# Optimization experiments

Measured on AMD Instinct MI355X. Metric: run time of the kernel, lower is better.

## Reference

```python
import jax, jax.numpy as jnp
import numpy as np

N_NODES = 50000
N_EDGES = 400000
D = 300          # num_features == hidden_units
L = 5            # num_layers
C = 128          # num_outputs
NG = 256         # graphs per batch
BN_EPS = 1e-5


def setup_inputs() -> dict:
    key = jax.random.key(0)
    ks = jax.random.split(key, 16)
    x = jax.random.normal(ks[0], (N_NODES, D), dtype=jnp.float32)
    edge_index = jax.random.randint(ks[1], (2, N_EDGES), 0, N_NODES, dtype=jnp.int64)
    batch = jnp.sort(jax.random.randint(ks[2], (N_NODES,), 0, NG, dtype=jnp.int64))
    s = 1.0 / np.sqrt(D)
    # Stacked per-layer GINConv MLP params: Linear -> BN -> ReLU -> Linear, then outer BN
    mlp_W1 = jax.random.uniform(ks[3], (L, D, D), jnp.float32, -s, s)
    mlp_b1 = jax.random.uniform(ks[4], (L, D), jnp.float32, -s, s)
    mlp_g1 = jnp.ones((L, D), jnp.float32)
    mlp_be1 = jnp.zeros((L, D), jnp.float32)
    mlp_W2 = jax.random.uniform(ks[5], (L, D, D), jnp.float32, -s, s)
    mlp_b2 = jax.random.uniform(ks[6], (L, D), jnp.float32, -s, s)
    bn_g = jnp.ones((L, D), jnp.float32)
    bn_b = jnp.zeros((L, D), jnp.float32)
    # num_layers+1 readout heads (num_features == hidden_units so all [D, C])
    fc_W = jax.random.uniform(ks[7], (L + 1, D, C), jnp.float32, -s, s)
    fc_b = jax.random.uniform(ks[8], (L + 1, C), jnp.float32, -s, s)
    return dict(x=x, edge_index=edge_index, batch=batch,
                mlp_W1=mlp_W1, mlp_b1=mlp_b1, mlp_g1=mlp_g1, mlp_be1=mlp_be1,
                mlp_W2=mlp_W2, mlp_b2=mlp_b2, bn_g=bn_g, bn_b=bn_b,
                fc_W=fc_W, fc_b=fc_b)


def _bn(h, gamma, beta):
    # BatchNorm1d in training mode: biased batch stats over the node dim
    mu = h.mean(axis=0)
    var = h.var(axis=0)
    return (h - mu) * jax.lax.rsqrt(var + BN_EPS) * gamma + beta


def reference(x, edge_index, batch, mlp_W1, mlp_b1, mlp_g1, mlp_be1,
              mlp_W2, mlp_b2, bn_g, bn_b, fc_W, fc_b):
    src, dst = edge_index[0], edge_index[1]
    n = x.shape[0]
    outs = [x]
    h = x
    for i in range(L):
        # GINConv (eps=0): MLP(x + sum_{j in N(i)} x_j), scatter-add over edges
        agg = jax.ops.segment_sum(h[src], dst, num_segments=n)
        z = h + agg
        z = z @ mlp_W1[i] + mlp_b1[i]
        z = jax.nn.relu(_bn(z, mlp_g1[i], mlp_be1[i]))
        z = z @ mlp_W2[i] + mlp_b2[i]
        h = jax.nn.relu(_bn(z, bn_g[i], bn_b[i]))  # outer BN + ReLU
        outs.append(h)
    # global mean pool per graph, then per-depth linear heads summed (dropout off in eval)
    counts = jax.ops.segment_sum(jnp.ones((n,), x.dtype), batch, num_segments=NG)
    inv = 1.0 / jnp.maximum(counts, 1.0)
    out = jnp.zeros((NG, C), x.dtype)
    for i, hi in enumerate(outs):
        pooled = jax.ops.segment_sum(hi, batch, num_segments=NG) * inv[:, None]
        out = out + (pooled @ fc_W[i] + fc_b[i])
    return out
```

## Files before the change

kernel.cpp:

```cpp
#include <hip/hip_runtime.h>

#define D 300
#define KP 320
#define NPAD 50048
#define NT128 391
#define WSTRIDE 328
#define NGR 256
#define NL 5
#define NC 128
#define SPART 8
#define BN_EPS 1e-5f

typedef __attribute__((ext_vector_type(8))) short bf16x8;
typedef __attribute__((ext_vector_type(4))) float f32x4;
typedef unsigned short u16;

__device__ __forceinline__ void atomAdd(float* p, float v) { unsafeAtomicAdd(p, v); }

__device__ __forceinline__ short f2bf(float f) {
    union { float f; unsigned u; } v; v.f = f;
    unsigned r = v.u + 0x7fffu + ((v.u >> 16) & 1u);
    return (short)(r >> 16);
}
__device__ __forceinline__ float bf2f(short s) {
    union { unsigned u; float f; } v;
    v.u = ((unsigned)(u16)s) << 16;
    return v.f;
}
__device__ __forceinline__ unsigned cvtpk(float lo, float hi) {
    unsigned r;
    asm("v_cvt_pk_bf16_f32 %0, %1, %2" : "=v"(r) : "v"(lo), "v"(hi));
    return r;
}
template<int C>
__device__ __forceinline__ float rs_add(float v) {
    int x = __builtin_amdgcn_update_dpp(0, __float_as_int(v), C, 0xF, 0xF, true);
    return v + __int_as_float(x);
}
__device__ __forceinline__ float red16(float v) {
    v = rs_add<0x111>(v);
    v = rs_add<0x112>(v);
    v = rs_add<0x114>(v);
    v = rs_add<0x118>(v);
    return v;
}

__global__ void offsets_kernel(const int* __restrict__ batch, int* __restrict__ off, int N) {
    int g = threadIdx.x;
    if (g > NGR) return;
    int lo = 0, hi = N;
    while (lo < hi) {
        int mid = (lo + hi) >> 1;
        if (batch[mid] < g) lo = mid + 1; else hi = mid;
    }
    off[g] = lo;
}

__global__ __launch_bounds__(256)
void deg_kernel(const int* __restrict__ ei, int* __restrict__ deg, int E) {
    int e = blockIdx.x * 256 + threadIdx.x;
    if (e < E) atomicAdd(&deg[ei[E + e]], 1);
}

__global__ __launch_bounds__(256)
void degpart_kernel(const int* __restrict__ deg, int* __restrict__ part, int N) {
    int i = blockIdx.x * 256 + threadIdx.x;
    int v = (i < N) ? deg[i] : 0;
    #pragma unroll
    for (int o = 1; o < 64; o <<= 1) v += __shfl_xor(v, o);
    __shared__ int ws[4];
    if ((threadIdx.x & 63) == 0) ws[threadIdx.x >> 6] = v;
    __syncthreads();
    if (threadIdx.x == 0) part[blockIdx.x] = ws[0] + ws[1] + ws[2] + ws[3];
}

__global__ __launch_bounds__(256)
void partscan_kernel(int* __restrict__ part, int nb) {
    __shared__ int buf[256];
    int t = threadIdx.x;
    int v = (t < nb) ? part[t] : 0;
    buf[t] = v;
    __syncthreads();
    for (int o = 1; o < 256; o <<= 1) {
        int u = (t >= o) ? buf[t - o] : 0;
        __syncthreads();
        buf[t] += u;
        __syncthreads();
    }
    if (t < nb) part[t] = (t == 0) ? 0 : buf[t - 1];
}

__global__ __launch_bounds__(256)
void rowptr_kernel(const int* __restrict__ deg, const int* __restrict__ part,
                   int* __restrict__ rowptr, int N, int E) {
    __shared__ int buf[256];
    int b = blockIdx.x, t = threadIdx.x;
    int i = b * 256 + t;
    int v = (i < N) ? deg[i] : 0;
    buf[t] = v;
    __syncthreads();
    for (int o = 1; o < 256; o <<= 1) {
        int u = (t >= o) ? buf[t - o] : 0;
        __syncthreads();
        buf[t] += u;
        __syncthreads();
    }
    if (i < N) rowptr[i] = part[b] + buf[t] - v;
    if (b == 0 && t == 0) rowptr[N] = E;
}

__global__ __launch_bounds__(256)
void fill_kernel(const int* __restrict__ ei, const int* __restrict__ rowptr,
                 int* __restrict__ cursor, int* __restrict__ col, int E) {
    int e = blockIdx.x * 256 + threadIdx.x;
    if (e >= E) return;
    int src = ei[e];
    int dst = ei[E + e];
    int pos = atomicAdd(&cursor[dst], 1);
    col[rowptr[dst] + pos] = src;
}

__global__ __launch_bounds__(256)
void wcvt_kernel(const float* __restrict__ W1, const float* __restrict__ W2,
                 u16* __restrict__ Wt) {
    int idx = blockIdx.x * 256 + threadIdx.x;
    if (idx >= 10 * KP * 80) return;
    int n4 = idx % 80;
    int k = (idx / 80) % KP;
    int mat = idx / (80 * KP);
    const float* Wsrc = (mat < NL) ? (W1 + (size_t)mat * D * D) : (W2 + (size_t)(mat - NL) * D * D);
    float4 w = make_float4(0.f, 0.f, 0.f, 0.f);
    if (k < D && n4 < 75) w = *(const float4*)(Wsrc + (size_t)k * D + n4 * 4);
    size_t base = ((size_t)mat * 320 + n4 * 4) * KP + k;
    Wt[base]          = (u16)f2bf(w.x);
    Wt[base + KP]     = (u16)f2bf(w.y);
    Wt[base + 2 * KP] = (u16)f2bf(w.z);
    Wt[base + 3 * KP] = (u16)f2bf(w.w);
}

__global__ __launch_bounds__(256)
void xcvt_kernel(const float* __restrict__ x, u16* __restrict__ xbf, int N) {
    int idx = blockIdx.x * 256 + threadIdx.x;
    if (idx >= NPAD * 40) return;
    int row = idx / 40;
    int c8 = (idx - row * 40) * 8;
    short o[8];
    #pragma unroll
    for (int i = 0; i < 8; ++i) {
        int c = c8 + i;
        float f = (row < N && c < D) ? x[(size_t)row * D + c] : 0.f;
        o[i] = f2bf(f);
    }
    *(bf16x8*)(xbf + (size_t)row * KP + c8) = *(bf16x8*)o;
}

template<bool APPLY>
__global__ __launch_bounds__(256)
void gather_kernel(const u16* __restrict__ H, u16* __restrict__ Z,
                   const int* __restrict__ rowptr, const int* __restrict__ col,
                   const float* __restrict__ scsh, int N) {
    int idx = blockIdx.x * 256 + threadIdx.x;
    if (idx >= N * 40) return;
    int node = idx / 40;
    int c8 = (idx - node * 40) * 8;
    float sc[8], sh[8];
    if (APPLY) {
        #pragma unroll
        for (int i = 0; i < 8; ++i) { sc[i] = scsh[c8 + i]; sh[i] = scsh[KP + c8 + i]; }
    }
    int s = rowptr[node], e = rowptr[node + 1];
    bf16x8 v = *(const bf16x8*)(H + (size_t)node * KP + c8);
    float acc[8];
    #pragma unroll
    for (int i = 0; i < 8; ++i) {
        float f = bf2f(v[i]);
        acc[i] = APPLY ? fmaxf(fmaf(f, sc[i], sh[i]), 0.f) : f;
    }
    int j = s;
    for (; j + 2 <= e; j += 2) {
        int s0 = col[j], s1 = col[j + 1];
        bf16x8 w0 = *(const bf16x8*)(H + (size_t)s0 * KP + c8);
        bf16x8 w1 = *(const bf16x8*)(H + (size_t)s1 * KP + c8);
        #pragma unroll
        for (int i = 0; i < 8; ++i) {
            float f0 = bf2f(w0[i]);
            float f1 = bf2f(w1[i]);
            acc[i] += APPLY ? fmaxf(fmaf(f0, sc[i], sh[i]), 0.f) : f0;
            acc[i] += APPLY ? fmaxf(fmaf(f1, sc[i], sh[i]), 0.f) : f1;
        }
    }
    if (j < e) {
        int s0 = col[j];
        bf16x8 w0 = *(const bf16x8*)(H + (size_t)s0 * KP + c8);
        #pragma unroll
        for (int i = 0; i < 8; ++i) {
            float f0 = bf2f(w0[i]);
            acc[i] += APPLY ? fmaxf(fmaf(f0, sc[i], sh[i]), 0.f) : f0;
        }
    }
    short o[8];
    #pragma unroll
    for (int i = 0; i < 8; ++i) o[i] = f2bf(acc[i]);
    *(bf16x8*)(Z + (size_t)node * KP + c8) = *(bf16x8*)o;
}

template<bool APPLY>
__global__ __launch_bounds__(320)
void pool_kernel(const u16* __restrict__ H, const int* __restrict__ off,
                 const float* __restrict__ scsh, float* __restrict__ pooled_l) {
    __shared__ float red[8][KP];
    int t = threadIdx.x;
    int g = blockIdx.x;
    int rq = t / 40;
    int c8 = (t - rq * 40) * 8;
    float sc[8], sh[8];
    if (APPLY) {
        #pragma unroll
        for (int i = 0; i < 8; ++i) { sc[i] = scsh[c8 + i]; sh[i] = scsh[KP + c8 + i]; }
    }
    int r0 = off[g], r1 = off[g + 1];
    float a[8] = {};
    for (int r = r0 + rq; r < r1; r += 8) {
        bf16x8 v = *(const bf16x8*)(H + (size_t)r * KP + c8);
        #pragma unroll
        for (int i = 0; i < 8; ++i) {
            float f = bf2f(v[i]);
            a[i] += APPLY ? fmaxf(fmaf(f, sc[i], sh[i]), 0.f) : f;
        }
    }
    #pragma unroll
    for (int i = 0; i < 8; ++i) red[rq][c8 + i] = a[i];
    __syncthreads();
    int c = t;
    if (c < D) {
        float s = 0.f;
        #pragma unroll
        for (int j = 0; j < 8; ++j) s += red[j][c];
        pooled_l[g * D + c] = s;
    }
}

template<bool APPLY>
__global__ __launch_bounds__(256, 3)
void mfma_gemm_kernel(const u16* __restrict__ Abf, const u16* __restrict__ Wt,
                      const float* __restrict__ scsh,
                      u16* __restrict__ Cbf, float* __restrict__ stats, int Nreal) {
    __shared__ u16 Ws[80 * WSTRIDE];
    __shared__ float lsum[80], lsq[80];
    const int tid = threadIdx.x;
    const int bid = blockIdx.x;
    const int xcd = bid & 7;
    const int pos = bid >> 3;
    const int tile = xcd + ((pos >> 2) << 3);
    const int nBase = (pos & 3) * 80;
    if (tile >= NT128) return;
    const int wave = tid >> 6, lane = tid & 63;
    const int quad = lane >> 4, l16 = lane & 15;

    const u16* pA = Abf + (size_t)(tile * 128 + wave * 16 + l16) * KP + quad * 8;
    bf16x8 a[2][10];
    #pragma unroll
    for (int kc = 0; kc < 10; ++kc) {
        a[0][kc] = *(const bf16x8*)(pA + kc * 32);
        a[1][kc] = *(const bf16x8*)(pA + (size_t)64 * KP + kc * 32);
    }

    {
        const u16* src = Wt + (size_t)nBase * KP;
        for (int unit = tid; unit < 80 * 40; unit += 256) {
            int n = unit / 40, kg = unit - n * 40;
            int kc = kg >> 2, q = kg & 3;
            *(bf16x8*)&Ws[n * WSTRIDE + kc * 32 + ((q ^ (n & 3)) << 3)] =
                *(const bf16x8*)(src + (size_t)n * KP + kg * 8);
        }
    }
    if (tid < 80) { lsum[tid] = 0.f; lsq[tid] = 0.f; }

    #pragma unroll
    for (int kc = 0; kc < 10; ++kc) {
        asm volatile("" : "+v"(a[0][kc]));
        asm volatile("" : "+v"(a[1][kc]));
    }
    __syncthreads();

    if (APPLY) {
        #pragma unroll
        for (int kc = 0; kc < 10; ++kc) {
            const float* sp = scsh + kc * 32 + quad * 8;
            float4 s0 = *(const float4*)sp;
            float4 s1 = *(const float4*)(sp + 4);
            float4 h0 = *(const float4*)(sp + KP);
            float4 h1 = *(const float4*)(sp + KP + 4);
            float sc[8] = {s0.x, s0.y, s0.z, s0.w, s1.x, s1.y, s1.z, s1.w};
            float sh[8] = {h0.x, h0.y, h0.z, h0.w, h1.x, h1.y, h1.z, h1.w};
            #pragma unroll
            for (int g = 0; g < 2; ++g) {
                float f[8];
                #pragma unroll
                for (int i = 0; i < 8; ++i)
                    f[i] = fmaxf(fmaf(bf2f(a[g][kc][i]), sc[i], sh[i]), 0.f);
                union { unsigned u[4]; bf16x8 v; } o;
                o.u[0] = cvtpk(f[0], f[1]);
                o.u[1] = cvtpk(f[2], f[3]);
                o.u[2] = cvtpk(f[4], f[5]);
                o.u[3] = cvtpk(f[6], f[7]);
                a[g][kc] = o.v;
            }
        }
    }

    int wb[5];
    #pragma unroll
    for (int nt = 0; nt < 5; ++nt)
        wb[nt] = (nt * 16 + l16) * WSTRIDE + ((quad ^ (l16 & 3)) << 3);

    f32x4 acc[2][5] = {};
    __builtin_amdgcn_s_setprio(1);
    #pragma unroll
    for (int kc = 0; kc < 10; ++kc) {
        #pragma unroll
        for (int nt = 0; nt < 5; ++nt) {
            bf16x8 b = *(const bf16x8*)&Ws[wb[nt] + kc * 32];
            acc[0][nt] = __builtin_amdgcn_mfma_f32_16x16x32_bf16(b, a[0][kc], acc[0][nt], 0, 0, 0);
            acc[1][nt] = __builtin_amdgcn_mfma_f32_16x16x32_bf16(b, a[1][kc], acc[1][nt], 0, 0, 0);
        }
    }
    __builtin_amdgcn_s_setprio(0);

    const int r0g = tile * 128 + wave * 16 + l16;
    const bool ok0 = r0g < Nreal, ok1 = (r0g + 64) < Nreal;
    u16* crow0 = Cbf + (size_t)r0g * KP + nBase + quad * 4;
    u16* crow1 = crow0 + (size_t)64 * KP;
    #pragma unroll
    for (int nt = 0; nt < 5; ++nt) {
        float v0[4], v1[4];
        #pragma unroll
        for (int r = 0; r < 4; ++r) { v0[r] = acc[0][nt][r]; v1[r] = acc[1][nt][r]; }
        uint2 w0, w1;
        w0.x = cvtpk(v0[0], v0[1]); w0.y = cvtpk(v0[2], v0[3]);
        w1.x = cvtpk(v1[0], v1[1]); w1.y = cvtpk(v1[2], v1[3]);
        *(uint2*)(crow0 + nt * 16) = w0;
        *(uint2*)(crow1 + nt * 16) = w1;
        #pragma unroll
        for (int r = 0; r < 4; ++r) {
            float s0 = ok0 ? v0[r] : 0.f;
            float s1 = ok1 ? v1[r] : 0.f;
            float sv = red16(s0 + s1);
            float qv = red16(fmaf(s0, s0, s1 * s1));
            if (l16 == 15) {
                atomicAdd(&lsum[nt * 16 + quad * 4 + r], sv);
                atomicAdd(&lsq [nt * 16 + quad * 4 + r], qv);
            }
        }
    }
    __syncthreads();
    if (tid < 80) {
        int colg = nBase + tid;
        if (colg < D) {
            float* sp = stats + (size_t)(bid & (SPART - 1)) * 2 * KP;
            atomAdd(&sp[colg], lsum[tid]);
            atomAdd(&sp[KP + colg], lsq[tid]);
        }
    }
}

__global__ void bnfin_kernel(float* __restrict__ sums, const float* __restrict__ g,
                             const float* __restrict__ be, float* __restrict__ scsh, float invN) {
    int c = threadIdx.x;
    if (c >= D) return;
    float t1 = 0.f, t2 = 0.f;
    #pragma unroll
    for (int p = 0; p < SPART; ++p) {
        t1 += sums[(size_t)p * 2 * KP + c];
        t2 += sums[(size_t)p * 2 * KP + KP + c];
        sums[(size_t)p * 2 * KP + c] = 0.f;
        sums[(size_t)p * 2 * KP + KP + c] = 0.f;
    }
    float mu = t1 * invN;
    float var = t2 * invN - mu * mu;
    float s = g[c] / sqrtf(var + BN_EPS);
    scsh[c] = s;
    scsh[KP + c] = fmaf(-mu, s, be[c]);
}

__global__ __launch_bounds__(128)
void bias_init_kernel(const float* __restrict__ fcb, float* __restrict__ out) {
    int i = blockIdx.x * 128 + threadIdx.x;
    if (i >= NGR * NC) return;
    int c = i & (NC - 1);
    float s = 0.f;
    for (int l = 0; l <= NL; ++l) s += fcb[l * NC + c];
    out[i] = s;
}

__global__ __launch_bounds__(128)
void readout_kernel(const float* __restrict__ pooled, const int* __restrict__ off,
                    const float* __restrict__ fcW, float* __restrict__ out) {
    __shared__ float sp[4][D];
    int c = threadIdx.x;
    int l = blockIdx.y;
    int g0 = blockIdx.x * 4;
    for (int i = c; i < 4 * D; i += 128) {
        int gg = i / D, k = i - gg * D;
        sp[gg][k] = pooled[((size_t)l * NGR + g0 + gg) * D + k];
    }
    __syncthreads();
    float acc[4] = {0.f, 0.f, 0.f, 0.f};
    for (int k = 0; k < D; ++k) {
        float w = fcW[((size_t)l * D + k) * NC + c];
        #pragma unroll
        for (int gg = 0; gg < 4; ++gg) acc[gg] = fmaf(sp[gg][k], w, acc[gg]);
    }
    #pragma unroll
    for (int gg = 0; gg < 4; ++gg) {
        int g = g0 + gg;
        float inv = 1.0f / fmaxf((float)(off[g + 1] - off[g]), 1.0f);
        atomAdd(&out[g * NC + c], acc[gg] * inv);
    }
}

extern "C" void kernel_launch(void* const* d_in, const int* in_sizes, int n_in,
                              void* d_out, int out_size, void* d_ws, size_t ws_size,
                              hipStream_t stream) {
    const float* x       = (const float*)d_in[0];
    const int*   ei      = (const int*)d_in[1];
    const int*   batch   = (const int*)d_in[2];
    const float* W1  = (const float*)d_in[3];
    const float* g1  = (const float*)d_in[5];
    const float* be1 = (const float*)d_in[6];
    const float* W2  = (const float*)d_in[7];
    const float* bng = (const float*)d_in[9];
    const float* bnb = (const float*)d_in[10];
    const float* fcW = (const float*)d_in[11];
    const float* fcb = (const float*)d_in[12];
    float* out = (float*)d_out;

    const int N = in_sizes[0] / D;
    const int E = in_sizes[1] / 2;
    const int nb = (N + 255) / 256;

    u16* xbf  = (u16*)d_ws;
    u16* bufA = xbf + (size_t)NPAD * KP;
    u16* bufB = bufA + (size_t)NPAD * KP;
    u16* Wt   = bufB + (size_t)NPAD * KP;
    float* pooled = (float*)(Wt + (size_t)10 * 320 * KP);
    float* stats  = pooled + (size_t)(NL + 1) * NGR * D;
    float* sc1    = stats + (size_t)SPART * 2 * KP;
    float* sc2    = sc1 + 2 * KP;
    int*   off    = (int*)(sc2 + 2 * KP);
    int*   rowptr = off + NGR + 1;
    int*   cursor = rowptr + N + 1;
    int*   col    = cursor + N;
    int*   part   = col + E;

    hipMemsetAsync(stats, 0, (SPART * 2 + 4) * KP * sizeof(float), stream);
    offsets_kernel<<<1, 320, 0, stream>>>(batch, off, N);
    bias_init_kernel<<<(NGR * NC + 127) / 128, 128, 0, stream>>>(fcb, out);

    hipMemsetAsync(cursor, 0, N * sizeof(int), stream);
    deg_kernel<<<(E + 255) / 256, 256, 0, stream>>>(ei, cursor, E);
    degpart_kernel<<<nb, 256, 0, stream>>>(cursor, part, N);
    partscan_kernel<<<1, 256, 0, stream>>>(part, nb);
    rowptr_kernel<<<nb, 256, 0, stream>>>(cursor, part, rowptr, N, E);
    hipMemsetAsync(cursor, 0, N * sizeof(int), stream);
    fill_kernel<<<(E + 255) / 256, 256, 0, stream>>>(ei, rowptr, cursor, col, E);

    wcvt_kernel<<<(10 * KP * 80 + 255) / 256, 256, 0, stream>>>(W1, W2, Wt);
    xcvt_kernel<<<(NPAD * 40 + 255) / 256, 256, 0, stream>>>(x, xbf, N);

    const int gemm_blocks = 8 * 49 * 4;
    const int nd40 = N * 40;
    float invN = 1.0f / (float)N;
    const size_t WtM = (size_t)320 * KP;

    pool_kernel<false><<<NGR, 320, 0, stream>>>(xbf, off, sc2, pooled);

    u16* g = bufA;
    u16* t = bufB;
    const u16* src = xbf;
    for (int l = 0; l < NL; ++l) {
        if (l == 0)
            gather_kernel<false><<<(nd40 + 255) / 256, 256, 0, stream>>>(src, g, rowptr, col, sc2, N);
        else
            gather_kernel<true><<<(nd40 + 255) / 256, 256, 0, stream>>>(src, g, rowptr, col, sc2, N);
        mfma_gemm_kernel<false><<<gemm_blocks, 256, 0, stream>>>(
            g, Wt + (size_t)l * WtM, sc1, t, stats, N);
        bnfin_kernel<<<1, 320, 0, stream>>>(stats, g1 + l * D, be1 + l * D, sc1, invN);
        mfma_gemm_kernel<true><<<gemm_blocks, 256, 0, stream>>>(
            t, Wt + (size_t)(NL + l) * WtM, sc1, g, stats, N);
        bnfin_kernel<<<1, 320, 0, stream>>>(stats, bng + l * D, bnb + l * D, sc2, invN);
        pool_kernel<true><<<NGR, 320, 0, stream>>>(g, off, sc2, pooled + (size_t)(l + 1) * NGR * D);
        src = g;
        u16* tmp = g; g = t; t = tmp;
    }
    readout_kernel<<<dim3(NGR / 4, NL + 1), 128, 0, stream>>>(pooled, off, fcW, out);
}
```

Before: 938.2 us.

## Share weight tile across two row tiles and replace stats atomics with partials

Each GEMM block now has 512 threads covering two 128-row tiles. Both tiles share one LDS-staged 80-column weight slice, which halves the weight staging per row tile and reduces the grid to 800 blocks. BatchNorm sum and sum-of-squares are no longer built with LDS and global atomics. Each wave writes per-slot partials into a scratch buffer aliased onto the x workspace, and bnfin reduces these with one block per column. In exchange the launch bound of 512 threads with 6 blocks may squeeze registers, out-of-range tiles still load A rows past valid data, and the psum alias depends on xbf being dead after layer 0's gather.

```diff
diff --git a/kernel.cpp b/kernel.cpp
--- a/kernel.cpp
+++ b/kernel.cpp
@@ -4,11 +4,12 @@
 #define KP 320
 #define NPAD 50048
 #define NT128 391
+#define NPAIR 200
+#define PSL 1600
 #define WSTRIDE 328
 #define NGR 256
 #define NL 5
 #define NC 128
-#define SPART 8
 #define BN_EPS 1e-5f
 
 typedef __attribute__((ext_vector_type(8))) short bf16x8;
@@ -241,23 +242,24 @@
 }
 
 template<bool APPLY>
-__global__ __launch_bounds__(256, 3)
+__global__ __launch_bounds__(512, 6)
 void mfma_gemm_kernel(const u16* __restrict__ Abf, const u16* __restrict__ Wt,
                       const float* __restrict__ scsh,
-                      u16* __restrict__ Cbf, float* __restrict__ stats, int Nreal) {
+                      u16* __restrict__ Cbf, float* __restrict__ psum, int Nreal) {
     __shared__ u16 Ws[80 * WSTRIDE];
-    __shared__ float lsum[80], lsq[80];
     const int tid = threadIdx.x;
     const int bid = blockIdx.x;
     const int xcd = bid & 7;
     const int pos = bid >> 3;
-    const int tile = xcd + ((pos >> 2) << 3);
+    const int pair = xcd + ((pos >> 2) << 3);
     const int nBase = (pos & 3) * 80;
-    if (tile >= NT128) return;
     const int wave = tid >> 6, lane = tid & 63;
+    const int wgrp = wave >> 2, wid = wave & 3;
     const int quad = lane >> 4, l16 = lane & 15;
-
-    const u16* pA = Abf + (size_t)(tile * 128 + wave * 16 + l16) * KP + quad * 8;
+    const int tile = 2 * pair + wgrp;
+    const bool live = tile < NT128;
+
+    const u16* pA = Abf + (size_t)(tile * 128 + wid * 16 + l16) * KP + quad * 8;
     bf16x8 a[2][10];
     #pragma unroll
     for (int kc = 0; kc < 10; ++kc) {
@@ -267,14 +269,13 @@
 
     {
         const u16* src = Wt + (size_t)nBase * KP;
-        for (int unit = tid; unit < 80 * 40; unit += 256) {
+        for (int unit = tid; unit < 80 * 40; unit += 512) {
             int n = unit / 40, kg = unit - n * 40;
             int kc = kg >> 2, q = kg & 3;
             *(bf16x8*)&Ws[n * WSTRIDE + kc * 32 + ((q ^ (n & 3)) << 3)] =
                 *(const bf16x8*)(src + (size_t)n * KP + kg * 8);
         }
     }
-    if (tid < 80) { lsum[tid] = 0.f; lsq[tid] = 0.f; }
 
     #pragma unroll
     for (int kc = 0; kc < 10; ++kc) {
@@ -327,20 +328,24 @@
     }
     __builtin_amdgcn_s_setprio(0);
 
-    const int r0g = tile * 128 + wave * 16 + l16;
+    const int r0g = tile * 128 + wid * 16 + l16;
     const bool ok0 = r0g < Nreal, ok1 = (r0g + 64) < Nreal;
     u16* crow0 = Cbf + (size_t)r0g * KP + nBase + quad * 4;
     u16* crow1 = crow0 + (size_t)64 * KP;
+    const int pslot = pair * 8 + wave;
+    float* psq = psum + (size_t)320 * PSL;
     #pragma unroll
     for (int nt = 0; nt < 5; ++nt) {
         float v0[4], v1[4];
         #pragma unroll
         for (int r = 0; r < 4; ++r) { v0[r] = acc[0][nt][r]; v1[r] = acc[1][nt][r]; }
-        uint2 w0, w1;
-        w0.x = cvtpk(v0[0], v0[1]); w0.y = cvtpk(v0[2], v0[3]);
-        w1.x = cvtpk(v1[0], v1[1]); w1.y = cvtpk(v1[2], v1[3]);
-        *(uint2*)(crow0 + nt * 16) = w0;
-        *(uint2*)(crow1 + nt * 16) = w1;
+        if (live) {
+            uint2 w0, w1;
+            w0.x = cvtpk(v0[0], v0[1]); w0.y = cvtpk(v0[2], v0[3]);
+            w1.x = cvtpk(v1[0], v1[1]); w1.y = cvtpk(v1[2], v1[3]);
+            *(uint2*)(crow0 + nt * 16) = w0;
+            *(uint2*)(crow1 + nt * 16) = w1;
+        }
         #pragma unroll
         for (int r = 0; r < 4; ++r) {
             float s0 = ok0 ? v0[r] : 0.f;
@@ -348,39 +353,37 @@
             float sv = red16(s0 + s1);
             float qv = red16(fmaf(s0, s0, s1 * s1));
             if (l16 == 15) {
-                atomicAdd(&lsum[nt * 16 + quad * 4 + r], sv);
-                atomicAdd(&lsq [nt * 16 + quad * 4 + r], qv);
+                int c = nBase + nt * 16 + quad * 4 + r;
+                psum[(size_t)c * PSL + pslot] = sv;
+                psq [(size_t)c * PSL + pslot] = qv;
             }
         }
     }
-    __syncthreads();
-    if (tid < 80) {
-        int colg = nBase + tid;
-        if (colg < D) {
-            float* sp = stats + (size_t)(bid & (SPART - 1)) * 2 * KP;
-            atomAdd(&sp[colg], lsum[tid]);
-            atomAdd(&sp[KP + colg], lsq[tid]);
-        }
-    }
-}
-
-__global__ void bnfin_kernel(float* __restrict__ sums, const float* __restrict__ g,
-                             const float* __restrict__ be, float* __restrict__ scsh, float invN) {
-    int c = threadIdx.x;
-    if (c >= D) return;
-    float t1 = 0.f, t2 = 0.f;
-    #pragma unroll
-    for (int p = 0; p < SPART; ++p) {
-        t1 += sums[(size_t)p * 2 * KP + c];
-        t2 += sums[(size_t)p * 2 * KP + KP + c];
-        sums[(size_t)p * 2 * KP + c] = 0.f;
-        sums[(size_t)p * 2 * KP + KP + c] = 0.f;
-    }
-    float mu = t1 * invN;
-    float var = t2 * invN - mu * mu;
-    float s = g[c] / sqrtf(var + BN_EPS);
-    scsh[c] = s;
-    scsh[KP + c] = fmaf(-mu, s, be[c]);
+}
+
+__global__ __launch_bounds__(256)
+void bnfin_kernel(const float* __restrict__ psum, const float* __restrict__ g,
+                  const float* __restrict__ be, float* __restrict__ scsh, float invN) {
+    int c = blockIdx.x;
+    const float* ps = psum + (size_t)c * PSL;
+    const float* pq = psum + (size_t)(320 + c) * PSL;
+    float s1 = 0.f, s2 = 0.f;
+    for (int i = threadIdx.x; i < PSL; i += 256) { s1 += ps[i]; s2 += pq[i]; }
+    #pragma unroll
+    for (int o = 1; o < 64; o <<= 1) { s1 += __shfl_xor(s1, o); s2 += __shfl_xor(s2, o); }
+    __shared__ float w1[4], w2[4];
+    int wv = threadIdx.x >> 6;
+    if ((threadIdx.x & 63) == 0) { w1[wv] = s1; w2[wv] = s2; }
+    __syncthreads();
+    if (threadIdx.x == 0) {
+        float t1 = w1[0] + w1[1] + w1[2] + w1[3];
+        float t2 = w2[0] + w2[1] + w2[2] + w2[3];
+        float mu = t1 * invN;
+        float var = t2 * invN - mu * mu;
+        float s = g[c] / sqrtf(var + BN_EPS);
+        scsh[c] = s;
+        scsh[KP + c] = fmaf(-mu, s, be[c]);
+    }
 }
 
 __global__ __launch_bounds__(128)
@@ -440,12 +443,12 @@
     const int nb = (N + 255) / 256;
 
     u16* xbf  = (u16*)d_ws;
+    float* psum = (float*)d_ws;
     u16* bufA = xbf + (size_t)NPAD * KP;
     u16* bufB = bufA + (size_t)NPAD * KP;
     u16* Wt   = bufB + (size_t)NPAD * KP;
     float* pooled = (float*)(Wt + (size_t)10 * 320 * KP);
-    float* stats  = pooled + (size_t)(NL + 1) * NGR * D;
-    float* sc1    = stats + (size_t)SPART * 2 * KP;
+    float* sc1    = pooled + (size_t)(NL + 1) * NGR * D;
     float* sc2    = sc1 + 2 * KP;
     int*   off    = (int*)(sc2 + 2 * KP);
     int*   rowptr = off + NGR + 1;
@@ -453,7 +456,7 @@
     int*   col    = cursor + N;
     int*   part   = col + E;
 
-    hipMemsetAsync(stats, 0, (SPART * 2 + 4) * KP * sizeof(float), stream);
+    hipMemsetAsync(sc1, 0, 4 * KP * sizeof(float), stream);
     offsets_kernel<<<1, 320, 0, stream>>>(batch, off, N);
     bias_init_kernel<<<(NGR * NC + 127) / 128, 128, 0, stream>>>(fcb, out);
 
@@ -468,7 +471,7 @@
     wcvt_kernel<<<(10 * KP * 80 + 255) / 256, 256, 0, stream>>>(W1, W2, Wt);
     xcvt_kernel<<<(NPAD * 40 + 255) / 256, 256, 0, stream>>>(x, xbf, N);
 
-    const int gemm_blocks = 8 * 49 * 4;
+    const int gemm_blocks = 8 * 100;
     const int nd40 = N * 40;
     float invN = 1.0f / (float)N;
     const size_t WtM = (size_t)320 * KP;
@@ -483,12 +486,12 @@
             gather_kernel<false><<<(nd40 + 255) / 256, 256, 0, stream>>>(src, g, rowptr, col, sc2, N);
         else
             gather_kernel<true><<<(nd40 + 255) / 256, 256, 0, stream>>>(src, g, rowptr, col, sc2, N);
-        mfma_gemm_kernel<false><<<gemm_blocks, 256, 0, stream>>>(
-            g, Wt + (size_t)l * WtM, sc1, t, stats, N);
-        bnfin_kernel<<<1, 320, 0, stream>>>(stats, g1 + l * D, be1 + l * D, sc1, invN);
-        mfma_gemm_kernel<true><<<gemm_blocks, 256, 0, stream>>>(
-            t, Wt + (size_t)(NL + l) * WtM, sc1, g, stats, N);
-        bnfin_kernel<<<1, 320, 0, stream>>>(stats, bng + l * D, bnb + l * D, sc2, invN);
+        mfma_gemm_kernel<false><<<gemm_blocks, 512, 0, stream>>>(
+            g, Wt + (size_t)l * WtM, sc1, t, psum, N);
+        bnfin_kernel<<<D, 256, 0, stream>>>(psum, g1 + l * D, be1 + l * D, sc1, invN);
+        mfma_gemm_kernel<true><<<gemm_blocks, 512, 0, stream>>>(
+            t, Wt + (size_t)(NL + l) * WtM, sc1, g, psum, N);
+        bnfin_kernel<<<D, 256, 0, stream>>>(psum, bng + l * D, bnb + l * D, sc2, invN);
         pool_kernel<true><<<NGR, 320, 0, stream>>>(g, off, sc2, pooled + (size_t)(l + 1) * NGR * D);
         src = g;
         u16* tmp = g; g = t; t = tmp;
```

New measurement: 1.373 ms. 1.46x slower.
